# Optimization experiments

Hardware: AMD Instinct MI355X
Metric: run time of the kernel (lower is better)

Reference implementation:

```python
import jax, jax.numpy as jnp
import numpy as np

N_EDGES = 1_600_000
N_NODES = 50_000
D_FEAT = 32


def setup_inputs() -> dict:
    key = jax.random.key(0)
    k_src, k_idx = jax.random.split(key)
    src = jax.random.normal(k_src, (N_EDGES, D_FEAT), dtype=jnp.float32)
    index = jax.random.randint(k_idx, (N_EDGES,), 0, N_NODES, dtype=jnp.int64 if jax.config.jax_enable_x64 else jnp.int32)
    out = jnp.zeros((N_NODES, D_FEAT), dtype=jnp.float32)
    return {"src": src, "index": index, "out": out}


def reference(src, index, out):
    # scatter_add(src, index, dim=0, out=out): out[index[e], :] += src[e, :]
    # Equivalent to out + segment_sum over the edge dim.
    return out + jax.ops.segment_sum(src, index, num_segments=out.shape[0])
```

## Files before the change

### kernel.cpp

```cpp
#include <hip/hip_runtime.h>

#define N_EDGES 1600000
#define N_NODES 50000
#define D_FEAT  32

#define BSHIFT  6
#define NPB     64
#define NB      ((N_NODES + NPB - 1) / NPB)
#define CHUNK   2048
#define NBLK    ((N_EDGES + CHUNK - 1) / CHUNK)
#define EPT     (CHUNK / 256)
#define MAXB    6144

#define BLKCNT_OFF 0
#define START_OFF  ((((size_t)NBLK * NB * 4 + 255) / 256) * 256)
#define PB_OFF     (START_OFF + ((((size_t)(NB + 1) * 4 + 255) / 256) * 256))
#define WS_NEEDED  (PB_OFF + (size_t)N_EDGES * 4)

__global__ __launch_bounds__(256) void count_kernel(const int* __restrict__ index,
                                                    int* __restrict__ blockcnt) {
    __shared__ int lcnt[NB];
    int t = threadIdx.x;
    for (int k = t; k < NB; k += 256) lcnt[k] = 0;
    __syncthreads();
    int base = blockIdx.x * CHUNK;
    #pragma unroll
    for (int j = 0; j < EPT; ++j) {
        int e = base + j * 256 + t;
        if (e < N_EDGES) atomicAdd(&lcnt[index[e] >> BSHIFT], 1);
    }
    __syncthreads();
    for (int k = t; k < NB; k += 256)
        blockcnt[(size_t)blockIdx.x * NB + k] = lcnt[k];
}

__global__ __launch_bounds__(256) void scan_col_kernel(int* __restrict__ blockcnt,
                                                       int* __restrict__ startg) {
    int wid  = (blockIdx.x * 256 + threadIdx.x) >> 6;
    int lane = threadIdx.x & 63;
    if (wid >= NB) return;
    int carry = 0;
    const int CH = (NBLK + 63) / 64;
    for (int c = 0; c < CH; ++c) {
        int b = c * 64 + lane;
        int v = (b < NBLK) ? blockcnt[(size_t)b * NB + wid] : 0;
        int incl = v;
        #pragma unroll
        for (int d = 1; d < 64; d <<= 1) {
            int up = __shfl_up(incl, d, 64);
            if (lane >= d) incl += up;
        }
        if (b < NBLK) blockcnt[(size_t)b * NB + wid] = carry + incl - v;
        carry += __shfl(incl, 63, 64);
    }
    if (lane == 0) startg[wid] = carry;
}

__global__ __launch_bounds__(1024) void scan_bucket_kernel(int* __restrict__ startg) {
    __shared__ int part[1024];
    int t = threadIdx.x;
    int v = (t < NB) ? startg[t] : 0;
    part[t] = v;
    __syncthreads();
    int inc = v;
    for (int d = 1; d < 1024; d <<= 1) {
        int w = (t >= d) ? part[t - d] : 0;
        __syncthreads();
        inc += w;
        part[t] = inc;
        __syncthreads();
    }
    if (t < NB) startg[t] = inc - v;
    if (t == 0) startg[NB] = N_EDGES;
}

__global__ __launch_bounds__(256) void partition_kernel(const int* __restrict__ index,
                                                        const int* __restrict__ blockcnt,
                                                        const int* __restrict__ startg,
                                                        int* __restrict__ pb) {
    __shared__ int lcnt[NB];
    __shared__ int loff[NB];
    __shared__ int lbase[NB];
    __shared__ int scanp[256];
    __shared__ int2 stage[CHUNK];
    int t = threadIdx.x;
    int b = blockIdx.x;
    for (int k = t; k < NB; k += 256) lcnt[k] = 0;
    __syncthreads();
    int base = b * CHUNK;
    int nd[EPT], rk[EPT];
    #pragma unroll
    for (int j = 0; j < EPT; ++j) {
        int e = base + j * 256 + t;
        nd[j] = -1;
        if (e < N_EDGES) {
            nd[j] = index[e];
            rk[j] = atomicAdd(&lcnt[nd[j] >> BSHIFT], 1);
        }
    }
    __syncthreads();
    {
        const int C = (NB + 255) / 256;
        int mybase = t * C;
        int s = 0;
        #pragma unroll
        for (int j = 0; j < C; ++j) {
            int i = mybase + j;
            if (i < NB) s += lcnt[i];
        }
        scanp[t] = s;
        __syncthreads();
        int inc = s;
        for (int d = 1; d < 256; d <<= 1) {
            int w = (t >= d) ? scanp[t - d] : 0;
            __syncthreads();
            inc += w;
            scanp[t] = inc;
            __syncthreads();
        }
        int run = inc - s;
        #pragma unroll
        for (int j = 0; j < C; ++j) {
            int i = mybase + j;
            if (i < NB) { loff[i] = run; run += lcnt[i]; }
        }
    }
    for (int k = t; k < NB; k += 256)
        lbase[k] = startg[k] + blockcnt[(size_t)b * NB + k];
    __syncthreads();
    #pragma unroll
    for (int j = 0; j < EPT; ++j) {
        if (nd[j] >= 0) {
            int e = base + j * 256 + t;
            int k = nd[j] >> BSHIFT;
            stage[loff[k] + rk[j]] = make_int2(nd[j], e);
        }
    }
    __syncthreads();
    int total = loff[NB - 1] + lcnt[NB - 1];
    for (int i = t; i < total; i += 256) {
        int2 ent = stage[i];
        int k = ent.x >> BSHIFT;
        pb[lbase[k] + (i - loff[k])] = (ent.y << BSHIFT) | (ent.x & (NPB - 1));
    }
}

__global__ __launch_bounds__(512) void finish_gather_kernel(const int* __restrict__ pb,
                                                            const int* __restrict__ startg,
                                                            const float4* __restrict__ src4,
                                                            const float4* __restrict__ out_in4,
                                                            float4* __restrict__ out4) {
    __shared__ int lperm[MAXB];
    __shared__ int lcnt[NPB];
    __shared__ int lcur[NPB];
    __shared__ int loffs[NPB + 1];
    int t = threadIdx.x;
    int k = blockIdx.x;
    if (t < NPB) lcnt[t] = 0;
    __syncthreads();
    int s0 = startg[k], s1 = startg[k + 1];
    int cnt = s1 - s0;
    for (int i = t; i < cnt; i += 512)
        atomicAdd(&lcnt[pb[s0 + i] & (NPB - 1)], 1);
    __syncthreads();
    if (t == 0) {
        int run = 0;
        for (int n = 0; n < NPB; ++n) {
            loffs[n] = run;
            lcur[n] = run;
            run += lcnt[n];
        }
        loffs[NPB] = run;
    }
    __syncthreads();
    for (int i = t; i < cnt; i += 512) {
        int pv = pb[s0 + i];
        int r = atomicAdd(&lcur[pv & (NPB - 1)], 1);
        lperm[r] = pv >> BSHIFT;
    }
    __syncthreads();

    int wave = t >> 6, lane = t & 63;
    int slot = lane >> 3, f4 = lane & 7;
    for (int nl = wave; nl < NPB; nl += 8) {
        int gnode = k * NPB + nl;
        if (gnode >= N_NODES) break;
        int start = loffs[nl], end = loffs[nl + 1];
        float4 a0 = {0,0,0,0}, a1 = {0,0,0,0}, a2 = {0,0,0,0}, a3 = {0,0,0,0};
        int i = start + slot;
        for (; i + 24 < end; i += 32) {
            int e0 = lperm[i];
            int e1 = lperm[i + 8];
            int e2 = lperm[i + 16];
            int e3 = lperm[i + 24];
            float4 v0 = src4[(size_t)e0 * 8 + f4];
            float4 v1 = src4[(size_t)e1 * 8 + f4];
            float4 v2 = src4[(size_t)e2 * 8 + f4];
            float4 v3 = src4[(size_t)e3 * 8 + f4];
            a0.x += v0.x; a0.y += v0.y; a0.z += v0.z; a0.w += v0.w;
            a1.x += v1.x; a1.y += v1.y; a1.z += v1.z; a1.w += v1.w;
            a2.x += v2.x; a2.y += v2.y; a2.z += v2.z; a2.w += v2.w;
            a3.x += v3.x; a3.y += v3.y; a3.z += v3.z; a3.w += v3.w;
        }
        for (; i < end; i += 8) {
            int e0 = lperm[i];
            float4 v0 = src4[(size_t)e0 * 8 + f4];
            a0.x += v0.x; a0.y += v0.y; a0.z += v0.z; a0.w += v0.w;
        }
        a0.x += a1.x + a2.x + a3.x;
        a0.y += a1.y + a2.y + a3.y;
        a0.z += a1.z + a2.z + a3.z;
        a0.w += a1.w + a2.w + a3.w;
        for (int m = 8; m <= 32; m <<= 1) {
            a0.x += __shfl_xor(a0.x, m, 64);
            a0.y += __shfl_xor(a0.y, m, 64);
            a0.z += __shfl_xor(a0.z, m, 64);
            a0.w += __shfl_xor(a0.w, m, 64);
        }
        if (slot == 0) {
            size_t o = (size_t)gnode * 8 + f4;
            float4 bo = out_in4[o];
            bo.x += a0.x; bo.y += a0.y; bo.z += a0.z; bo.w += a0.w;
            out4[o] = bo;
        }
    }
}

__global__ void init_out_kernel(const float4* __restrict__ out_in,
                                float4* __restrict__ out, int n4) {
    int i = blockIdx.x * blockDim.x + threadIdx.x;
    int stride = gridDim.x * blockDim.x;
    for (; i < n4; i += stride) out[i] = out_in[i];
}
__global__ void scatter_direct_kernel(const float* __restrict__ src,
                                      const int* __restrict__ index,
                                      float* __restrict__ out) {
    const long total = (long)N_EDGES * D_FEAT;
    long i = (long)blockIdx.x * blockDim.x + threadIdx.x;
    const long stride = (long)gridDim.x * blockDim.x;
    for (; i < total; i += stride) {
        int e = (int)(i >> 5);
        int f = (int)(i & 31);
        float v = src[i];
        int node = index[e];
        atomicAdd(&out[(size_t)node * D_FEAT + f], v);
    }
}

extern "C" void kernel_launch(void* const* d_in, const int* in_sizes, int n_in,
                              void* d_out, int out_size, void* d_ws, size_t ws_size,
                              hipStream_t stream) {
    const float* src    = (const float*)d_in[0];
    const int*   index  = (const int*)d_in[1];
    const float* out_in = (const float*)d_in[2];
    float* out          = (float*)d_out;

    if (ws_size < WS_NEEDED) {
        int n4 = out_size / 4;
        init_out_kernel<<<1563, 256, 0, stream>>>((const float4*)out_in, (float4*)out, n4);
        scatter_direct_kernel<<<2048, 256, 0, stream>>>(src, index, out);
        return;
    }

    char* ws = (char*)d_ws;
    int* blockcnt = (int*)(ws + BLKCNT_OFF);
    int* startg   = (int*)(ws + START_OFF);
    int* pb       = (int*)(ws + PB_OFF);

    count_kernel<<<NBLK, 256, 0, stream>>>(index, blockcnt);
    scan_col_kernel<<<(NB * 64 + 255) / 256, 256, 0, stream>>>(blockcnt, startg);
    scan_bucket_kernel<<<1, 1024, 0, stream>>>(startg);
    partition_kernel<<<NBLK, 256, 0, stream>>>(index, blockcnt, startg, pb);
    finish_gather_kernel<<<NB, 512, 0, stream>>>(pb, startg, (const float4*)src,
                                                 (const float4*)out_in, (float4*)out);
}
```

Measured before the change: 77.22 us.

## Double partition chunk size, vectorize index loads, parallelize per-bucket node scan

```diff
diff --git a/kernel.cpp b/kernel.cpp
--- a/kernel.cpp
+++ b/kernel.cpp
@@ -7,9 +7,10 @@
 #define BSHIFT  6
 #define NPB     64
 #define NB      ((N_NODES + NPB - 1) / NPB)
-#define CHUNK   2048
+#define CHUNK   4096
 #define NBLK    ((N_EDGES + CHUNK - 1) / CHUNK)
 #define EPT     (CHUNK / 256)
+#define EPT4    (EPT / 4)
 #define MAXB    6144
 
 #define BLKCNT_OFF 0
@@ -17,17 +18,23 @@
 #define PB_OFF     (START_OFF + ((((size_t)(NB + 1) * 4 + 255) / 256) * 256))
 #define WS_NEEDED  (PB_OFF + (size_t)N_EDGES * 4)
 
-__global__ __launch_bounds__(256) void count_kernel(const int* __restrict__ index,
+__global__ __launch_bounds__(256) void count_kernel(const int4* __restrict__ index4,
                                                     int* __restrict__ blockcnt) {
     __shared__ int lcnt[NB];
     int t = threadIdx.x;
     for (int k = t; k < NB; k += 256) lcnt[k] = 0;
     __syncthreads();
-    int base = blockIdx.x * CHUNK;
+    int base4 = blockIdx.x * (CHUNK / 4);
     #pragma unroll
-    for (int j = 0; j < EPT; ++j) {
-        int e = base + j * 256 + t;
-        if (e < N_EDGES) atomicAdd(&lcnt[index[e] >> BSHIFT], 1);
+    for (int j = 0; j < EPT4; ++j) {
+        int e4 = base4 + j * 256 + t;
+        if (e4 < N_EDGES / 4) {
+            int4 v = index4[e4];
+            atomicAdd(&lcnt[v.x >> BSHIFT], 1);
+            atomicAdd(&lcnt[v.y >> BSHIFT], 1);
+            atomicAdd(&lcnt[v.z >> BSHIFT], 1);
+            atomicAdd(&lcnt[v.w >> BSHIFT], 1);
+        }
     }
     __syncthreads();
     for (int k = t; k < NB; k += 256)
@@ -74,7 +81,7 @@
     if (t == 0) startg[NB] = N_EDGES;
 }
 
-__global__ __launch_bounds__(256) void partition_kernel(const int* __restrict__ index,
+__global__ __launch_bounds__(256) void partition_kernel(const int4* __restrict__ index4,
                                                         const int* __restrict__ blockcnt,
                                                         const int* __restrict__ startg,
                                                         int* __restrict__ pb) {
@@ -87,15 +94,19 @@
     int b = blockIdx.x;
     for (int k = t; k < NB; k += 256) lcnt[k] = 0;
     __syncthreads();
-    int base = b * CHUNK;
+    int base4 = b * (CHUNK / 4);
     int nd[EPT], rk[EPT];
     #pragma unroll
-    for (int j = 0; j < EPT; ++j) {
-        int e = base + j * 256 + t;
-        nd[j] = -1;
-        if (e < N_EDGES) {
-            nd[j] = index[e];
-            rk[j] = atomicAdd(&lcnt[nd[j] >> BSHIFT], 1);
+    for (int j = 0; j < EPT4; ++j) {
+        int e4 = base4 + j * 256 + t;
+        if (e4 < N_EDGES / 4) {
+            int4 v = index4[e4];
+            nd[j * 4 + 0] = v.x; rk[j * 4 + 0] = atomicAdd(&lcnt[v.x >> BSHIFT], 1);
+            nd[j * 4 + 1] = v.y; rk[j * 4 + 1] = atomicAdd(&lcnt[v.y >> BSHIFT], 1);
+            nd[j * 4 + 2] = v.z; rk[j * 4 + 2] = atomicAdd(&lcnt[v.z >> BSHIFT], 1);
+            nd[j * 4 + 3] = v.w; rk[j * 4 + 3] = atomicAdd(&lcnt[v.w >> BSHIFT], 1);
+        } else {
+            nd[j * 4 + 0] = nd[j * 4 + 1] = nd[j * 4 + 2] = nd[j * 4 + 3] = -1;
         }
     }
     __syncthreads();
@@ -131,7 +142,8 @@
     #pragma unroll
     for (int j = 0; j < EPT; ++j) {
         if (nd[j] >= 0) {
-            int e = base + j * 256 + t;
+            int e4 = base4 + (j >> 2) * 256 + t;
+            int e = e4 * 4 + (j & 3);
             int k = nd[j] >> BSHIFT;
             stage[loff[k] + rk[j]] = make_int2(nd[j], e);
         }
@@ -163,14 +175,17 @@
     for (int i = t; i < cnt; i += 512)
         atomicAdd(&lcnt[pb[s0 + i] & (NPB - 1)], 1);
     __syncthreads();
-    if (t == 0) {
-        int run = 0;
-        for (int n = 0; n < NPB; ++n) {
-            loffs[n] = run;
-            lcur[n] = run;
-            run += lcnt[n];
-        }
-        loffs[NPB] = run;
+    if (t < NPB) {
+        int v = lcnt[t];
+        int inc = v;
+        #pragma unroll
+        for (int d = 1; d < 64; d <<= 1) {
+            int up = __shfl_up(inc, d, 64);
+            if (t >= d) inc += up;
+        }
+        loffs[t] = inc - v;
+        lcur[t]  = inc - v;
+        if (t == NPB - 1) loffs[NPB] = inc;
     }
     __syncthreads();
     for (int i = t; i < cnt; i += 512) {
@@ -267,10 +282,10 @@
     int* startg   = (int*)(ws + START_OFF);
     int* pb       = (int*)(ws + PB_OFF);
 
-    count_kernel<<<NBLK, 256, 0, stream>>>(index, blockcnt);
+    count_kernel<<<NBLK, 256, 0, stream>>>((const int4*)index, blockcnt);
     scan_col_kernel<<<(NB * 64 + 255) / 256, 256, 0, stream>>>(blockcnt, startg);
     scan_bucket_kernel<<<1, 1024, 0, stream>>>(startg);
-    partition_kernel<<<NBLK, 256, 0, stream>>>(index, blockcnt, startg, pb);
+    partition_kernel<<<NBLK, 256, 0, stream>>>((const int4*)index, blockcnt, startg, pb);
     finish_gather_kernel<<<NB, 512, 0, stream>>>(pb, startg, (const float4*)src,
                                                  (const float4*)out_in, (float4*)out);
 }
```

Result: faster. 68.79 us (-10.9%).
